# Optimization experiments

Hardware: AMD Instinct MI355X
Metric: run time of the kernel (lower is better)

## Reference

```python
import jax, jax.numpy as jnp
import numpy as np

B, T, F, H = 512, 512, 32, 64  # batch, lag, n_features, hidden_sizes[0]


def _lstm_layer(x_seq, Wih, Whh, bih, bhh):
    """Single LSTM layer, batch_first input [B,T,Fin] -> [B,T,H].
    PyTorch gate order: i, f, g, o."""
    # Precompute input projections for all timesteps (one big GEMM)
    xg = jnp.einsum('btf,gf->btg', x_seq, Wih) + bih + bhh  # [B,T,4H]
    xg_t = jnp.transpose(xg, (1, 0, 2))  # [T,B,4H]
    h0 = jnp.zeros((x_seq.shape[0], Whh.shape[1]), x_seq.dtype)
    c0 = jnp.zeros_like(h0)

    def step(carry, g_t):
        h, c = carry
        gates = g_t + h @ Whh.T  # [B,4H]
        i, f, g, o = jnp.split(gates, 4, axis=-1)
        i = jax.nn.sigmoid(i)
        f = jax.nn.sigmoid(f)
        g = jnp.tanh(g)
        o = jax.nn.sigmoid(o)
        c = f * c + i * g
        h = o * jnp.tanh(c)
        return (h, c), h

    (_, _), hs = jax.lax.scan(step, (h0, c0), xg_t)  # hs: [T,B,H]
    return jnp.transpose(hs, (1, 0, 2))  # [B,T,H]


def setup_inputs() -> dict:
    key = jax.random.key(0)
    ks = jax.random.split(key, 12)
    s_in = 1.0 / np.sqrt(H)
    u = lambda k, shape: jax.random.uniform(k, shape, jnp.float32, -s_in, s_in)
    return {
        'x': jax.random.normal(ks[0], (B, T, F), jnp.float32),
        'Wih0': u(ks[1], (4 * H, F)),
        'Whh0': u(ks[2], (4 * H, H)),
        'bih0': u(ks[3], (4 * H,)),
        'bhh0': u(ks[4], (4 * H,)),
        'Wih1': u(ks[5], (4 * H, H)),
        'Whh1': u(ks[6], (4 * H, H)),
        'bih1': u(ks[7], (4 * H,)),
        'bhh1': u(ks[8], (4 * H,)),
        'fcW': u(ks[9], (1, H)),
        'fcb': u(ks[10], (1,)),
    }


def reference(x, Wih0, Whh0, bih0, bhh0, Wih1, Whh1, bih1, bhh1, fcW, fcb):
    h1 = _lstm_layer(x, Wih0, Whh0, bih0, bhh0)   # [B,T,H]
    h2 = _lstm_layer(h1, Wih1, Whh1, bih1, bhh1)  # [B,T,H]  (dropout=0 at inference)
    last = h2[:, -1, :]                           # [B,H]
    out = last @ fcW.T + fcb                      # [B,1]
    return out.squeeze(-1)                        # [B]
```

## Files before the change

kernel.cpp:

```cpp
#include <hip/hip_runtime.h>
#include <math.h>

#define Bsz 512
#define Tsz 512
#define Fin 32
#define Hd 64
#define CHUNK 32
#define NCH (Tsz / CHUNK)

typedef float v2f __attribute__((ext_vector_type(2)));

__device__ __forceinline__ float fsig(float x) {
    return __builtin_amdgcn_rcpf(1.0f + __expf(-x));
}
__device__ __forceinline__ float ftanh(float x) {
    return fmaf(2.0f, __builtin_amdgcn_rcpf(1.0f + __expf(-2.0f * x)), -1.0f);
}

#define PIN4(v4) \
    asm volatile("" : "+v"((v4).x), "+v"((v4).y), "+v"((v4).z), "+v"((v4).w))

__global__ __launch_bounds__(256, 2)
void lstm_layer0(const float* __restrict__ x,
                 const float4* __restrict__ Wih4,
                 const float4* __restrict__ Whh4,
                 const float* __restrict__ bih,
                 const float* __restrict__ bhh,
                 float* __restrict__ h1out)
{
    __shared__ __align__(16) float xbuf[2][CHUNK * Fin];
    __shared__ __align__(16) float hcopy[4][Hd];
    __shared__ float glds[2][Hd * 5];

    const int tid  = threadIdx.x;
    const int lane = tid & 63;
    const int wv   = tid >> 6;
    const int wvu  = __builtin_amdgcn_readfirstlane(wv);
    const int b    = blockIdx.x;

    float4 wih[8];
#pragma unroll
    for (int q = 0; q < 8; ++q) wih[q] = Wih4[tid * 8 + q];
    float4 whh[16];
#pragma unroll
    for (int q = 0; q < 16; ++q) whh[q] = Whh4[tid * 16 + q];
    float bias = bih[tid] + bhh[tid];

    float c = 0.0f;
    hcopy[wv][lane] = 0.0f;

    const float4* xsrc = (const float4*)(x + (size_t)b * Tsz * Fin);
    ((float4*)xbuf[0])[tid] = xsrc[tid];
    float* hout = h1out + (size_t)b * Tsz * Hd + lane;
    __syncthreads();

    for (int ci = 0; ci < NCH; ++ci) {
        const int cur = ci & 1;
        if (ci + 1 < NCH)
            ((float4*)xbuf[cur ^ 1])[tid] = xsrc[(ci + 1) * (CHUNK * Fin / 4) + tid];
#pragma unroll
        for (int q = 0; q < 8; ++q)  PIN4(wih[q]);
#pragma unroll
        for (int q = 0; q < 16; ++q) PIN4(whh[q]);
#pragma unroll 1
        for (int ct = 0; ct < CHUNK; ct += 2) {
#pragma unroll
            for (int pp = 0; pp < 2; ++pp) {
                const float4* xrow = (const float4*)&xbuf[cur][(ct + pp) * Fin];
                const float4* hrow = (const float4*)&hcopy[wv][0];

                v2f a0 = {bias, 0.0f};
                v2f a1 = {0.0f, 0.0f};
#pragma unroll
                for (int q = 0; q < 8; ++q) {
                    float4 xv = xrow[q];
                    v2f b0 = {xv.x, xv.y}, b1 = {xv.z, xv.w};
                    v2f w0 = {wih[q].x, wih[q].y}, w1 = {wih[q].z, wih[q].w};
                    a0 = __builtin_elementwise_fma(b0, w0, a0);
                    a1 = __builtin_elementwise_fma(b1, w1, a1);
                }
#pragma unroll
                for (int q = 0; q < 16; ++q) {
                    float4 hv = hrow[q];
                    v2f b0 = {hv.x, hv.y}, b1 = {hv.z, hv.w};
                    v2f w0 = {whh[q].x, whh[q].y}, w1 = {whh[q].z, whh[q].w};
                    a0 = __builtin_elementwise_fma(b0, w0, a0);
                    a1 = __builtin_elementwise_fma(b1, w1, a1);
                }
                float a = (a0.x + a0.y) + (a1.x + a1.y);
                if (wvu == 2) glds[pp][lane * 5 + wv] = ftanh(a);
                else          glds[pp][lane * 5 + wv] = fsig(a);
                __syncthreads();
                float gi = glds[pp][lane * 5 + 0];
                float gf = glds[pp][lane * 5 + 1];
                float gg = glds[pp][lane * 5 + 2];
                float go = glds[pp][lane * 5 + 3];
                c = fmaf(gf, c, gi * gg);
                float h = go * ftanh(c);
                hcopy[wv][lane] = h;
                if (wvu == 0)
                    hout[(size_t)(ci * CHUNK + ct + pp) * Hd] = h;
            }
        }
    }
}

__global__ __launch_bounds__(256, 2)
void lstm_layer1_fc(const float* __restrict__ h1,
                    const float4* __restrict__ Wih4,
                    const float4* __restrict__ Whh4,
                    const float* __restrict__ bih,
                    const float* __restrict__ bhh,
                    const float* __restrict__ fcW,
                    const float* __restrict__ fcb,
                    float* __restrict__ out)
{
    __shared__ __align__(16) float xbuf[2][CHUNK * Hd];
    __shared__ __align__(16) float hcopy[4][Hd];
    __shared__ float glds[2][Hd * 5];

    const int tid  = threadIdx.x;
    const int lane = tid & 63;
    const int wv   = tid >> 6;
    const int wvu  = __builtin_amdgcn_readfirstlane(wv);
    const int b    = blockIdx.x;

    float4 wih[16];
#pragma unroll
    for (int q = 0; q < 16; ++q) wih[q] = Wih4[tid * 16 + q];
    float4 whh[16];
#pragma unroll
    for (int q = 0; q < 16; ++q) whh[q] = Whh4[tid * 16 + q];
    float bias = bih[tid] + bhh[tid];

    float c  = 0.0f;
    float hl = 0.0f;
    hcopy[wv][lane] = 0.0f;

    const float4* xsrc = (const float4*)(h1 + (size_t)b * Tsz * Hd);
    ((float4*)xbuf[0])[tid]       = xsrc[tid];
    ((float4*)xbuf[0])[tid + 256] = xsrc[tid + 256];
    __syncthreads();

    for (int ci = 0; ci < NCH; ++ci) {
        const int cur = ci & 1;
        if (ci + 1 < NCH) {
            ((float4*)xbuf[cur ^ 1])[tid]       = xsrc[(ci + 1) * (CHUNK * Hd / 4) + tid];
            ((float4*)xbuf[cur ^ 1])[tid + 256] = xsrc[(ci + 1) * (CHUNK * Hd / 4) + tid + 256];
        }
#pragma unroll
        for (int q = 0; q < 16; ++q) PIN4(wih[q]);
#pragma unroll
        for (int q = 0; q < 16; ++q) PIN4(whh[q]);
#pragma unroll 1
        for (int ct = 0; ct < CHUNK; ct += 2) {
#pragma unroll
            for (int pp = 0; pp < 2; ++pp) {
                const float4* xrow = (const float4*)&xbuf[cur][(ct + pp) * Hd];
                const float4* hrow = (const float4*)&hcopy[wv][0];

                v2f a0 = {bias, 0.0f};
                v2f a1 = {0.0f, 0.0f};
#pragma unroll
                for (int q = 0; q < 16; ++q) {
                    float4 xv = xrow[q];
                    v2f b0 = {xv.x, xv.y}, b1 = {xv.z, xv.w};
                    v2f w0 = {wih[q].x, wih[q].y}, w1 = {wih[q].z, wih[q].w};
                    a0 = __builtin_elementwise_fma(b0, w0, a0);
                    a1 = __builtin_elementwise_fma(b1, w1, a1);
                }
#pragma unroll
                for (int q = 0; q < 16; ++q) {
                    float4 hv = hrow[q];
                    v2f b0 = {hv.x, hv.y}, b1 = {hv.z, hv.w};
                    v2f w0 = {whh[q].x, whh[q].y}, w1 = {whh[q].z, whh[q].w};
                    a0 = __builtin_elementwise_fma(b0, w0, a0);
                    a1 = __builtin_elementwise_fma(b1, w1, a1);
                }
                float a = (a0.x + a0.y) + (a1.x + a1.y);
                if (wvu == 2) glds[pp][lane * 5 + wv] = ftanh(a);
                else          glds[pp][lane * 5 + wv] = fsig(a);
                __syncthreads();
                float gi = glds[pp][lane * 5 + 0];
                float gf = glds[pp][lane * 5 + 1];
                float gg = glds[pp][lane * 5 + 2];
                float go = glds[pp][lane * 5 + 3];
                c  = fmaf(gf, c, gi * gg);
                hl = go * ftanh(c);
                hcopy[wv][lane] = hl;
            }
        }
    }
    if (wvu == 0) {
        float psum = hl * fcW[lane];
#pragma unroll
        for (int off = 32; off > 0; off >>= 1)
            psum += __shfl_down(psum, off);
        if (lane == 0) out[b] = psum + fcb[0];
    }
}

extern "C" void kernel_launch(void* const* d_in, const int* in_sizes, int n_in,
                              void* d_out, int out_size, void* d_ws, size_t ws_size,
                              hipStream_t stream)
{
    const float* x    = (const float*)d_in[0];
    const float* Wih0 = (const float*)d_in[1];
    const float* Whh0 = (const float*)d_in[2];
    const float* bih0 = (const float*)d_in[3];
    const float* bhh0 = (const float*)d_in[4];
    const float* Wih1 = (const float*)d_in[5];
    const float* Whh1 = (const float*)d_in[6];
    const float* bih1 = (const float*)d_in[7];
    const float* bhh1 = (const float*)d_in[8];
    const float* fcW  = (const float*)d_in[9];
    const float* fcb  = (const float*)d_in[10];
    float* out = (float*)d_out;
    float* h1  = (float*)d_ws;

    lstm_layer0<<<dim3(Bsz), dim3(256), 0, stream>>>(
        x, (const float4*)Wih0, (const float4*)Whh0, bih0, bhh0, h1);
    lstm_layer1_fc<<<dim3(Bsz), dim3(256), 0, stream>>>(
        h1, (const float4*)Wih1, (const float4*)Whh1, bih1, bhh1, fcW, fcb, out);
}
```

Before: 746.1 us.

## Hoist input projections into separate GEMM kernels and use single-wave recurrence

Splits each LSTM layer into two kernels. A batched GEMM first computes the input-to-gate projections plus biases for all timesteps into a workspace buffer. A recurrence kernel then runs with one 64-lane wave per batch element, each lane holding all four gate rows of Whh in registers, so the per-step __syncthreads and the LDS gate exchange go away. The trade-off is a large xg workspace (written and read once per layer) and lower occupancy; the old fused kernels remain as a fallback when the workspace is too small.

```diff
diff --git a/kernel.cpp b/kernel.cpp
--- a/kernel.cpp
+++ b/kernel.cpp
@@ -7,6 +7,8 @@
 #define Hd 64
 #define CHUNK 32
 #define NCH (Tsz / CHUNK)
+#define NG 256
+#define NBT (Bsz * Tsz)
 
 typedef float v2f __attribute__((ext_vector_type(2)));
 
@@ -20,13 +22,185 @@
 #define PIN4(v4) \
     asm volatile("" : "+v"((v4).x), "+v"((v4).y), "+v"((v4).z), "+v"((v4).w))
 
+
+template <int K>
 __global__ __launch_bounds__(256, 2)
-void lstm_layer0(const float* __restrict__ x,
-                 const float4* __restrict__ Wih4,
-                 const float4* __restrict__ Whh4,
-                 const float* __restrict__ bih,
-                 const float* __restrict__ bhh,
-                 float* __restrict__ h1out)
+void xg_gemm(const float* __restrict__ X,
+             const float4* __restrict__ W4,
+             const float* __restrict__ bih,
+             const float* __restrict__ bhh,
+             float* __restrict__ xg)
+{
+    __shared__ __align__(16) float xs[64 * K];
+    const int r    = threadIdx.x;
+    const int row0 = blockIdx.x * 64;
+
+    float4 w[K / 4];
+#pragma unroll
+    for (int j = 0; j < K / 4; ++j) w[j] = W4[r * (K / 4) + j];
+    const float bias = bih[r] + bhh[r];
+
+    const float4* xsrc = (const float4*)(X + (size_t)row0 * K);
+#pragma unroll
+    for (int i = 0; i < (64 * K / 4) / 256; ++i)
+        ((float4*)xs)[i * 256 + r] = xsrc[i * 256 + r];
+    __syncthreads();
+
+    float* dst = xg + (size_t)row0 * NG + r;
+#pragma unroll 1
+    for (int j = 0; j < 64; ++j) {
+        const float4* xp = (const float4*)&xs[j * K];
+        v2f a0 = {bias, 0.0f}, a1 = {0.0f, 0.0f};
+#pragma unroll
+        for (int k = 0; k < K / 4; ++k) {
+            float4 xv = xp[k];
+            v2f b0 = {xv.x, xv.y}, b1 = {xv.z, xv.w};
+            v2f w0 = {w[k].x, w[k].y}, w1 = {w[k].z, w[k].w};
+            a0 = __builtin_elementwise_fma(b0, w0, a0);
+            a1 = __builtin_elementwise_fma(b1, w1, a1);
+        }
+        dst[(size_t)j * NG] = (a0.x + a0.y) + (a1.x + a1.y);
+    }
+}
+
+#define REC_STEP(T, G0, G1, G2, G3, DO_STORE)                                 \
+    {                                                                         \
+        v2f a00 = {G0, 0.f}, a01 = {0.f, 0.f};                                \
+        v2f a10 = {G1, 0.f}, a11 = {0.f, 0.f};                                \
+        v2f a20 = {G2, 0.f}, a21 = {0.f, 0.f};                                \
+        v2f a30 = {G3, 0.f}, a31 = {0.f, 0.f};                                \
+        const int tpf = ((T) + 2 < Tsz) ? (T) + 2 : (Tsz - 1);                \
+        G0 = xgl[tpf * NG + 0];                                               \
+        G1 = xgl[tpf * NG + 64];                                              \
+        G2 = xgl[tpf * NG + 128];                                             \
+        G3 = xgl[tpf * NG + 192];                                             \
+        const float4* hv4 = (const float4*)hrow;                              \
+        _Pragma("unroll")                                                     \
+        for (int k = 0; k < 16; ++k) {                                        \
+            float4 hv = hv4[k];                                               \
+            v2f hb0 = {hv.x, hv.y}, hb1 = {hv.z, hv.w};                       \
+            v2f w00 = {whh[0][k].x, whh[0][k].y};                             \
+            v2f w01 = {whh[0][k].z, whh[0][k].w};                             \
+            v2f w10 = {whh[1][k].x, whh[1][k].y};                             \
+            v2f w11 = {whh[1][k].z, whh[1][k].w};                             \
+            v2f w20 = {whh[2][k].x, whh[2][k].y};                             \
+            v2f w21 = {whh[2][k].z, whh[2][k].w};                             \
+            v2f w30 = {whh[3][k].x, whh[3][k].y};                             \
+            v2f w31 = {whh[3][k].z, whh[3][k].w};                             \
+            a00 = __builtin_elementwise_fma(hb0, w00, a00);                   \
+            a01 = __builtin_elementwise_fma(hb1, w01, a01);                   \
+            a10 = __builtin_elementwise_fma(hb0, w10, a10);                   \
+            a11 = __builtin_elementwise_fma(hb1, w11, a11);                   \
+            a20 = __builtin_elementwise_fma(hb0, w20, a20);                   \
+            a21 = __builtin_elementwise_fma(hb1, w21, a21);                   \
+            a30 = __builtin_elementwise_fma(hb0, w30, a30);                   \
+            a31 = __builtin_elementwise_fma(hb1, w31, a31);                   \
+        }                                                                     \
+        float ai = (a00.x + a00.y) + (a01.x + a01.y);                         \
+        float af = (a10.x + a10.y) + (a11.x + a11.y);                         \
+        float ag = (a20.x + a20.y) + (a21.x + a21.y);                         \
+        float ao = (a30.x + a30.y) + (a31.x + a31.y);                         \
+        float gi = fsig(ai), gf = fsig(af);                                   \
+        float gg = ftanh(ag), go = fsig(ao);                                  \
+        c        = fmaf(gf, c, gi * gg);                                      \
+        hcur     = go * ftanh(c);                                             \
+        hrow[l]  = hcur;                                                      \
+        DO_STORE;                                                             \
+    }
+
+__global__ __launch_bounds__(64, 1)
+void lstm_rec0(const float4* __restrict__ Whh4,
+               const float* __restrict__ xg,
+               float* __restrict__ h1out)
+{
+    __shared__ __align__(16) float hrow[Hd];
+    const int l = threadIdx.x;
+    const int b = blockIdx.x;
+
+    float4 whh[4][16];
+#pragma unroll
+    for (int q = 0; q < 4; ++q)
+#pragma unroll
+        for (int j = 0; j < 16; ++j)
+            whh[q][j] = Whh4[(q * Hd + l) * 16 + j];
+
+    const float* xgl = xg + (size_t)b * Tsz * NG + l;
+    float* hout = h1out + (size_t)b * Tsz * Hd + l;
+
+    float c = 0.0f, hcur = 0.0f;
+    hrow[l] = 0.0f;
+
+    float gA0 = xgl[0], gA1 = xgl[64], gA2 = xgl[128], gA3 = xgl[192];
+    float gB0 = xgl[NG + 0], gB1 = xgl[NG + 64];
+    float gB2 = xgl[NG + 128], gB3 = xgl[NG + 192];
+
+    for (int ci = 0; ci < NCH; ++ci) {
+#pragma unroll
+        for (int q = 0; q < 4; ++q)
+#pragma unroll
+            for (int j = 0; j < 16; ++j) PIN4(whh[q][j]);
+#pragma unroll 1
+        for (int ct = 0; ct < CHUNK; ct += 2) {
+            const int t = ci * CHUNK + ct;
+            REC_STEP(t,     gA0, gA1, gA2, gA3, hout[(size_t)t * Hd] = hcur);
+            REC_STEP(t + 1, gB0, gB1, gB2, gB3, hout[(size_t)(t + 1) * Hd] = hcur);
+        }
+    }
+}
+
+__global__ __launch_bounds__(64, 1)
+void lstm_rec1_fc(const float4* __restrict__ Whh4,
+                  const float* __restrict__ xg,
+                  const float* __restrict__ fcW,
+                  const float* __restrict__ fcb,
+                  float* __restrict__ out)
+{
+    __shared__ __align__(16) float hrow[Hd];
+    const int l = threadIdx.x;
+    const int b = blockIdx.x;
+
+    float4 whh[4][16];
+#pragma unroll
+    for (int q = 0; q < 4; ++q)
+#pragma unroll
+        for (int j = 0; j < 16; ++j)
+            whh[q][j] = Whh4[(q * Hd + l) * 16 + j];
+
+    const float* xgl = xg + (size_t)b * Tsz * NG + l;
+
+    float c = 0.0f, hcur = 0.0f;
+    hrow[l] = 0.0f;
+
+    float gA0 = xgl[0], gA1 = xgl[64], gA2 = xgl[128], gA3 = xgl[192];
+    float gB0 = xgl[NG + 0], gB1 = xgl[NG + 64];
+    float gB2 = xgl[NG + 128], gB3 = xgl[NG + 192];
+
+    for (int ci = 0; ci < NCH; ++ci) {
+#pragma unroll
+        for (int q = 0; q < 4; ++q)
+#pragma unroll
+            for (int j = 0; j < 16; ++j) PIN4(whh[q][j]);
+#pragma unroll 1
+        for (int ct = 0; ct < CHUNK; ct += 2) {
+            const int t = ci * CHUNK + ct;
+            REC_STEP(t,     gA0, gA1, gA2, gA3, );
+            REC_STEP(t + 1, gB0, gB1, gB2, gB3, );
+        }
+    }
+    float psum = hcur * fcW[l];
+#pragma unroll
+    for (int off = 32; off > 0; off >>= 1)
+        psum += __shfl_down(psum, off);
+    if (l == 0) out[b] = psum + fcb[0];
+}
+
+__global__ __launch_bounds__(256, 2)
+void lstm_layer0_fb(const float* __restrict__ x,
+                    const float4* __restrict__ Wih4,
+                    const float4* __restrict__ Whh4,
+                    const float* __restrict__ bih,
+                    const float* __restrict__ bhh,
+                    float* __restrict__ h1out)
 {
     __shared__ __align__(16) float xbuf[2][CHUNK * Fin];
     __shared__ __align__(16) float hcopy[4][Hd];
@@ -67,10 +241,8 @@
 #pragma unroll
             for (int pp = 0; pp < 2; ++pp) {
                 const float4* xrow = (const float4*)&xbuf[cur][(ct + pp) * Fin];
-                const float4* hrow = (const float4*)&hcopy[wv][0];
-
-                v2f a0 = {bias, 0.0f};
-                v2f a1 = {0.0f, 0.0f};
+                const float4* hrw  = (const float4*)&hcopy[wv][0];
+                v2f a0 = {bias, 0.0f}, a1 = {0.0f, 0.0f};
 #pragma unroll
                 for (int q = 0; q < 8; ++q) {
                     float4 xv = xrow[q];
@@ -81,7 +253,7 @@
                 }
 #pragma unroll
                 for (int q = 0; q < 16; ++q) {
-                    float4 hv = hrow[q];
+                    float4 hv = hrw[q];
                     v2f b0 = {hv.x, hv.y}, b1 = {hv.z, hv.w};
                     v2f w0 = {whh[q].x, whh[q].y}, w1 = {whh[q].z, whh[q].w};
                     a0 = __builtin_elementwise_fma(b0, w0, a0);
@@ -106,14 +278,14 @@
 }
 
 __global__ __launch_bounds__(256, 2)
-void lstm_layer1_fc(const float* __restrict__ h1,
-                    const float4* __restrict__ Wih4,
-                    const float4* __restrict__ Whh4,
-                    const float* __restrict__ bih,
-                    const float* __restrict__ bhh,
-                    const float* __restrict__ fcW,
-                    const float* __restrict__ fcb,
-                    float* __restrict__ out)
+void lstm_layer1_fc_fb(const float* __restrict__ h1,
+                       const float4* __restrict__ Wih4,
+                       const float4* __restrict__ Whh4,
+                       const float* __restrict__ bih,
+                       const float* __restrict__ bhh,
+                       const float* __restrict__ fcW,
+                       const float* __restrict__ fcb,
+                       float* __restrict__ out)
 {
     __shared__ __align__(16) float xbuf[2][CHUNK * Hd];
     __shared__ __align__(16) float hcopy[4][Hd];
@@ -157,10 +329,8 @@
 #pragma unroll
             for (int pp = 0; pp < 2; ++pp) {
                 const float4* xrow = (const float4*)&xbuf[cur][(ct + pp) * Hd];
-                const float4* hrow = (const float4*)&hcopy[wv][0];
-
-                v2f a0 = {bias, 0.0f};
-                v2f a1 = {0.0f, 0.0f};
+                const float4* hrw  = (const float4*)&hcopy[wv][0];
+                v2f a0 = {bias, 0.0f}, a1 = {0.0f, 0.0f};
 #pragma unroll
                 for (int q = 0; q < 16; ++q) {
                     float4 xv = xrow[q];
@@ -171,7 +341,7 @@
                 }
 #pragma unroll
                 for (int q = 0; q < 16; ++q) {
-                    float4 hv = hrow[q];
+                    float4 hv = hrw[q];
                     v2f b0 = {hv.x, hv.y}, b1 = {hv.z, hv.w};
                     v2f w0 = {whh[q].x, whh[q].y}, w1 = {whh[q].z, whh[q].w};
                     a0 = __builtin_elementwise_fma(b0, w0, a0);
@@ -216,10 +386,26 @@
     const float* fcW  = (const float*)d_in[9];
     const float* fcb  = (const float*)d_in[10];
     float* out = (float*)d_out;
-    float* h1  = (float*)d_ws;
-
-    lstm_layer0<<<dim3(Bsz), dim3(256), 0, stream>>>(
-        x, (const float4*)Wih0, (const float4*)Whh0, bih0, bhh0, h1);
-    lstm_layer1_fc<<<dim3(Bsz), dim3(256), 0, stream>>>(
-        h1, (const float4*)Wih1, (const float4*)Whh1, bih1, bhh1, fcW, fcb, out);
-}
+
+    const size_t h1_bytes = (size_t)Bsz * Tsz * Hd * sizeof(float);
+    const size_t xg_bytes = (size_t)NBT * NG * sizeof(float);
+
+    if (ws_size >= h1_bytes + xg_bytes) {
+        float* h1 = (float*)d_ws;
+        float* xg = (float*)((char*)d_ws + h1_bytes);
+        xg_gemm<Fin><<<dim3(NBT / 64), dim3(256), 0, stream>>>(
+            x, (const float4*)Wih0, bih0, bhh0, xg);
+        lstm_rec0<<<dim3(Bsz), dim3(64), 0, stream>>>(
+            (const float4*)Whh0, xg, h1);
+        xg_gemm<Hd><<<dim3(NBT / 64), dim3(256), 0, stream>>>(
+            h1, (const float4*)Wih1, bih1, bhh1, xg);
+        lstm_rec1_fc<<<dim3(Bsz), dim3(64), 0, stream>>>(
+            (const float4*)Whh1, xg, fcW, fcb, out);
+    } else {
+        float* h1 = (float*)d_ws;
+        lstm_layer0_fb<<<dim3(Bsz), dim3(256), 0, stream>>>(
+            x, (const float4*)Wih0, (const float4*)Whh0, bih0, bhh0, h1);
+        lstm_layer1_fc_fb<<<dim3(Bsz), dim3(256), 0, stream>>>(
+            h1, (const float4*)Wih1, (const float4*)Whh1, bih1, bhh1, fcW, fcb, out);
+    }
+}
```

After: 743.4 us. No clear change (-0.4%).
